# Optimization experiments

Hardware: AMD Instinct MI355X
Metric: run time of the kernel (lower is better)

## Reference

```python
import jax, jax.numpy as jnp
import numpy as np
from jax import lax

B, S, T, E, H, V = 32, 64, 48, 512, 1024, 32000
PAD = 0


def lstm_cell(x, h, c, W_ih, W_hh, b_ih, b_hh):
    # PyTorch gate order: i, f, g, o
    gates = x @ W_ih.T + b_ih + h @ W_hh.T + b_hh
    i, f, g, o = jnp.split(gates, 4, axis=-1)
    c = jax.nn.sigmoid(f) * c + jax.nn.sigmoid(i) * jnp.tanh(g)
    h = jax.nn.sigmoid(o) * jnp.tanh(c)
    return h, c


def setup_inputs() -> dict:
    key = jax.random.key(0)
    ks = jax.random.split(key, 24)
    sc = 0.02
    n = lambda k, shape: jax.random.normal(k, shape, jnp.float32) * sc
    src_emb = n(ks[0], (V, E)).at[PAD].set(0.0)
    tgt_emb = n(ks[1], (V, E)).at[PAD].set(0.0)
    inp = {
        "input_sequences": jax.random.randint(ks[2], (B, S), 0, V),
        "target_sequences": jax.random.randint(ks[3], (B, T), 0, V),
        "src_emb": src_emb,
        "tgt_emb": tgt_emb,
        "enc_Wih_f": n(ks[4], (4 * H, E)),
        "enc_Whh_f": n(ks[5], (4 * H, H)),
        "enc_bih_f": n(ks[6], (4 * H,)),
        "enc_bhh_f": n(ks[7], (4 * H,)),
        "enc_Wih_b": n(ks[8], (4 * H, E)),
        "enc_Whh_b": n(ks[9], (4 * H, H)),
        "enc_bih_b": n(ks[10], (4 * H,)),
        "enc_bhh_b": n(ks[11], (4 * H,)),
        "dec_Wih": n(ks[12], (4 * H, E + H)),
        "dec_Whh": n(ks[13], (4 * H, H)),
        "dec_bih": n(ks[14], (4 * H,)),
        "dec_bhh": n(ks[15], (4 * H,)),
        "W_init_h": n(ks[16], (H, 2 * H)),
        "W_init_c": n(ks[17], (H, 2 * H)),
        "W_att": n(ks[18], (H, 2 * H)),
        "W_comb": n(ks[19], (H, 3 * H)),
        "W_proj": n(ks[20], (V, H)),
    }
    return inp


def reference(input_sequences, target_sequences, src_emb, tgt_emb,
              enc_Wih_f, enc_Whh_f, enc_bih_f, enc_bhh_f,
              enc_Wih_b, enc_Whh_b, enc_bih_b, enc_bhh_b,
              dec_Wih, dec_Whh, dec_bih, dec_bhh,
              W_init_h, W_init_c, W_att, W_comb, W_proj):
    bsz = input_sequences.shape[0]
    x_src = src_emb[input_sequences.T]  # (S, B, E) time-major

    def make_enc_step(W_ih, W_hh, b_ih, b_hh):
        def step(carry, x):
            h, c = carry
            h, c = lstm_cell(x, h, c, W_ih, W_hh, b_ih, b_hh)
            return (h, c), h
        return step

    h0 = jnp.zeros((bsz, H), x_src.dtype)
    c0 = jnp.zeros((bsz, H), x_src.dtype)
    # bidirectional encoder
    (hf, cf), hs_f = lax.scan(make_enc_step(enc_Wih_f, enc_Whh_f, enc_bih_f, enc_bhh_f), (h0, c0), x_src)
    (hb, cb), hs_b = lax.scan(make_enc_step(enc_Wih_b, enc_Whh_b, enc_bih_b, enc_bhh_b), (h0, c0), x_src[::-1])
    enc_h = jnp.concatenate([hs_f, hs_b[::-1]], axis=-1).transpose(1, 0, 2)  # (B, S, 2H)
    last_hidden = jnp.concatenate([hf, hb], axis=-1)  # (B, 2H)
    last_cell = jnp.concatenate([cf, cb], axis=-1)

    dec_h0 = last_hidden @ W_init_h.T
    dec_c0 = last_cell @ W_init_c.T
    enc_att = enc_h @ W_att.T  # (B, S, H)

    x_tgt = tgt_emb[target_sequences.T]  # (T, B, E)

    def dec_step(carry, e_t):
        h, c, prev_out = carry
        x = jnp.concatenate([e_t, prev_out], axis=-1)  # (B, E+H)
        h, c = lstm_cell(x, h, c, dec_Wih, dec_Whh, dec_bih, dec_bhh)
        scores = jnp.einsum('bh,bsh->bs', h, enc_att)
        attn = jax.nn.softmax(scores, axis=-1)
        ctx = jnp.einsum('bs,bsd->bd', attn, enc_h)  # (B, 2H)
        out = jnp.concatenate([h, ctx], axis=-1) @ W_comb.T  # (B, H)
        return (h, c, out), out

    prev0 = jnp.zeros((bsz, H), x_src.dtype)
    _, outs = lax.scan(dec_step, (dec_h0, dec_c0, prev0), x_tgt)  # (T, B, H)

    logits = outs @ W_proj.T  # (T, B, V)
    P = jax.nn.log_softmax(logits, axis=-1)
    tgt = target_sequences.T  # (T, B)
    # P[t] predicts tgt[t+1]; torch.gather with smaller index truncates P to T-1 steps
    gold = jnp.take_along_axis(P[:-1], tgt[1:][..., None], axis=-1)[..., 0]  # (T-1, B)
    scores = gold.sum(axis=0)  # (B,)
    return scores
```

## Files before the change

kernel.cpp:

```cpp
#include <hip/hip_runtime.h>

typedef short v8s __attribute__((ext_vector_type(8)));
typedef float v4f __attribute__((ext_vector_type(4)));
typedef unsigned short u16;

#define DI __device__ __forceinline__
#define MFMA(a, b, c) __builtin_amdgcn_mfma_f32_16x16x32_bf16(a, b, c, 0, 0, 0)

constexpr int B = 32, S = 64, T = 48, E = 512, H = 1024, V = 32000;
constexpr int TP = T - 1;
constexpr int MROWS = TP * B;
constexpr int NCH = 250;

DI u16 f2bf(float f) {
    unsigned u = __float_as_uint(f);
    unsigned r = (u + 0x7FFFu + ((u >> 16) & 1u)) >> 16;
    return (u16)r;
}
DI float bf2f(u16 h) { return __uint_as_float(((unsigned)h) << 16); }
DI v8s load8(const u16* p) { return *reinterpret_cast<const v8s*>(p); }

typedef __attribute__((address_space(1))) const unsigned int gu32;
typedef __attribute__((address_space(3))) unsigned int lu32;
DI void gload_lds16(const u16* g, u16* l) {
    __builtin_amdgcn_global_load_lds((gu32*)g, (lu32*)l, 16, 0, 0);
}

DI void cstore(unsigned* p, unsigned v) {
    __hip_atomic_store(p, v, __ATOMIC_RELAXED, __HIP_MEMORY_SCOPE_AGENT);
}
DI int cload(const int* p) {
    return __hip_atomic_load(p, __ATOMIC_RELAXED, __HIP_MEMORY_SCOPE_AGENT);
}

DI void gbar2(int* bar, int bid, int nblk, int v) {
    __syncthreads();
    if (bid == 0) {
        int t = threadIdx.x;
        if (t > 0 && t < nblk) {
            while (cload(bar + 16 + t * 4) < v) __builtin_amdgcn_s_sleep(1);
        }
        __syncthreads();
        if (t == 0)
            __hip_atomic_store(bar, v, __ATOMIC_RELAXED, __HIP_MEMORY_SCOPE_AGENT);
    } else {
        if (threadIdx.x == 0) {
            __hip_atomic_store(bar + 16 + bid * 4, v, __ATOMIC_RELAXED,
                               __HIP_MEMORY_SCOPE_AGENT);
            while (cload(bar) < v) __builtin_amdgcn_s_sleep(2);
        }
        __syncthreads();
    }
}

__global__ __launch_bounds__(256) void k_cvt(const float* __restrict__ s,
                                             u16* __restrict__ d, int n4) {
    int i = blockIdx.x * 256 + threadIdx.x;
    if (i >= n4) return;
    float4 v = reinterpret_cast<const float4*>(s)[i];
    ushort4 o;
    o.x = f2bf(v.x); o.y = f2bf(v.y); o.z = f2bf(v.z); o.w = f2bf(v.w);
    reinterpret_cast<ushort4*>(d)[i] = o;
}

struct CvtD {
    const float* src[11];
    u16* dst[11];
    int n4[11];
    int start[12];
};
__global__ __launch_bounds__(256) void k_cvtm(CvtD d) {
    int blk = blockIdx.x;
    int seg = 0;
    #pragma unroll
    for (int q = 0; q < 11; ++q)
        if (blk >= d.start[q + 1]) seg = q + 1;
    int i = (blk - d.start[seg]) * 256 + threadIdx.x;
    if (i >= d.n4[seg]) return;
    float4 v = reinterpret_cast<const float4*>(d.src[seg])[i];
    ushort4 o;
    o.x = f2bf(v.x); o.y = f2bf(v.y); o.z = f2bf(v.z); o.w = f2bf(v.w);
    reinterpret_cast<ushort4*>(d.dst[seg])[i] = o;
}

__global__ __launch_bounds__(256) void k_embed(const int* __restrict__ seq, int seqstr,
                                               int nsteps, const float* __restrict__ emb,
                                               u16* __restrict__ out) {
    int i = blockIdx.x * 256 + threadIdx.x;
    int total = nsteps * B * (E / 4);
    if (i >= total) return;
    int q = i & 127;
    int sb = i >> 7;
    int b = sb & 31;
    int s = sb >> 5;
    int tok = seq[b * seqstr + s];
    float4 v = reinterpret_cast<const float4*>(emb + (size_t)tok * E)[q];
    ushort4 o;
    o.x = f2bf(v.x); o.y = f2bf(v.y); o.z = f2bf(v.z); o.w = f2bf(v.w);
    reinterpret_cast<ushort4*>(out + ((size_t)(s * B + b)) * E)[q] = o;
}

__global__ __launch_bounds__(256) void k_ench(const u16* __restrict__ hsf,
                                              const u16* __restrict__ hsb,
                                              u16* __restrict__ ench) {
    int id = blockIdx.x * 256 + threadIdx.x;
    int d8 = id & 255; int s = (id >> 8) & 63; int b = id >> 14;
    int d0 = d8 * 8;
    const u16* src = (d0 < H) ? hsf + (((size_t)(s + 1) * B + b)) * H + d0
                              : hsb + (((size_t)(S - s) * B + b)) * H + (d0 - H);
    *reinterpret_cast<v8s*>(ench + ((size_t)b * S + s) * 2 * H + d0) = load8(src);
}

__global__ __launch_bounds__(256) void k_transp(const u16* __restrict__ in,
                                                u16* __restrict__ out, int K, int N) {
    __shared__ u16 t[64][72];
    int nt = blockIdx.x * 64, kt = blockIdx.y * 64;
    int tid = threadIdx.x;
    int r = tid >> 2, cq = (tid & 3) * 16;
    v8s v0 = load8(in + (size_t)(kt + r) * N + nt + cq);
    v8s v1 = load8(in + (size_t)(kt + r) * N + nt + cq + 8);
    #pragma unroll
    for (int e = 0; e < 8; ++e) { t[r][cq + e] = (u16)v0[e]; t[r][cq + 8 + e] = (u16)v1[e]; }
    __syncthreads();
    v8s o0, o1;
    #pragma unroll
    for (int e = 0; e < 8; ++e) { o0[e] = (short)t[cq + e][r]; o1[e] = (short)t[cq + 8 + e][r]; }
    *reinterpret_cast<v8s*>(out + (size_t)(nt + r) * K + kt + cq) = o0;
    *reinterpret_cast<v8s*>(out + (size_t)(nt + r) * K + kt + cq + 8) = o1;
}

__global__ __launch_bounds__(256) void k_tile(const u16* __restrict__ A, int astr,
                                              const u16* __restrict__ W, int wstr,
                                              float* __restrict__ outf,
                                              u16* __restrict__ outb, int ostr,
                                              int ktiles) {
    __shared__ __align__(16) u16 As[128 * 64];
    __shared__ __align__(16) u16 Bs[128 * 64];
    const int tid = threadIdx.x;
    const int lane = tid & 63, wv = tid >> 6;
    const int l15 = lane & 15, lg = lane >> 4;
    const int wr = wv >> 1, wc = wv & 1;
    const int m0 = blockIdx.y * 128, n0 = blockIdx.x * 128;
    const int srow = lane >> 3, sc_ = lane & 7;

    v4f acc[4][4];
    #pragma unroll
    for (int i = 0; i < 4; ++i)
        #pragma unroll
        for (int j = 0; j < 4; ++j) acc[i][j] = v4f{0.f, 0.f, 0.f, 0.f};

    for (int kt = 0; kt < ktiles; ++kt) {
        const int kb = kt * 64;
        #pragma unroll
        for (int i = 0; i < 4; ++i) {
            int chunk = wv * 4 + i;
            int row = chunk * 8 + srow;
            int csw = (sc_ ^ (row & 7)) << 3;
            gload_lds16(A + (size_t)(m0 + row) * astr + kb + csw, As + chunk * 512);
            gload_lds16(W + (size_t)(n0 + row) * wstr + kb + csw, Bs + chunk * 512);
        }
        __syncthreads();
        #pragma unroll
        for (int kk = 0; kk < 2; ++kk) {
            int sw = (((kk << 2) | lg) ^ (l15 & 7)) << 3;
            v8s af[4], bfv[4];
            #pragma unroll
            for (int mi = 0; mi < 4; ++mi)
                af[mi] = load8(As + (wr * 64 + mi * 16 + l15) * 64 + sw);
            #pragma unroll
            for (int ni = 0; ni < 4; ++ni)
                bfv[ni] = load8(Bs + (wc * 64 + ni * 16 + l15) * 64 + sw);
            #pragma unroll
            for (int mi = 0; mi < 4; ++mi)
                #pragma unroll
                for (int ni = 0; ni < 4; ++ni)
                    acc[mi][ni] = MFMA(af[mi], bfv[ni], acc[mi][ni]);
        }
        __syncthreads();
    }
    #pragma unroll
    for (int mi = 0; mi < 4; ++mi)
        #pragma unroll
        for (int rr = 0; rr < 4; ++rr) {
            int row = m0 + wr * 64 + mi * 16 + lg * 4 + rr;
            #pragma unroll
            for (int ni = 0; ni < 4; ++ni) {
                int col = n0 + wc * 64 + ni * 16 + l15;
                if (outf) outf[(size_t)row * ostr + col] = acc[mi][ni][rr];
                else      outb[(size_t)row * ostr + col] = f2bf(acc[mi][ni][rr]);
            }
        }
}

struct Seg { const u16* a; int astr; const u16* w; int wstr; int k; };

__global__ __launch_bounds__(512) void k_mm(Seg s1, Seg s2, float* __restrict__ outf,
                                            u16* __restrict__ outb, int ostr, int ks) {
    const int tid = threadIdx.x;
    const int wv = tid >> 6, lane = tid & 63;
    const int l15 = lane & 15, lg = lane >> 4;
    const int wrow = blockIdx.x * 16 + l15;
    const int k0 = wv * ks, k1 = k0 + ks;
    v4f acc0 = {0.f, 0.f, 0.f, 0.f}, acc1 = {0.f, 0.f, 0.f, 0.f};
    int base = 0;
    auto doseg = [&](const Seg& sg) {
        if (sg.k == 0) return;
        int s0 = k0 > base ? k0 : base;
        int send = base + sg.k;
        int s1e = k1 < send ? k1 : send;
        const u16* wp = sg.w + (size_t)wrow * sg.wstr + 8 * lg;
        const u16* a0p = sg.a + (size_t)l15 * sg.astr + 8 * lg;
        const u16* a1p = sg.a + (size_t)(16 + l15) * sg.astr + 8 * lg;
        #pragma unroll 2
        for (int k = s0; k < s1e; k += 32) {
            int kl = k - base;
            v8s bf = load8(wp + kl);
            v8s af0 = load8(a0p + kl);
            v8s af1 = load8(a1p + kl);
            acc0 = MFMA(af0, bf, acc0);
            acc1 = MFMA(af1, bf, acc1);
        }
        base += sg.k;
    };
    doseg(s1); doseg(s2);

    __shared__ float g[8][32][16];
    #pragma unroll
    for (int r = 0; r < 4; ++r) {
        g[wv][lg * 4 + r][l15] = acc0[r];
        g[wv][16 + lg * 4 + r][l15] = acc1[r];
    }
    __syncthreads();
    {
        int b = tid >> 4, cl = tid & 15;
        float v = 0.f;
        #pragma unroll
        for (int w = 0; w < 8; ++w) v += g[w][b][cl];
        int col = blockIdx.x * 16 + cl;
        if (outb) outb[(size_t)b * ostr + col] = f2bf(v);
        else      outf[(size_t)b * ostr + col] = v;
    }
}

__global__ __launch_bounds__(512) void k_enc(
    const float* __restrict__ xgF, const float* __restrict__ xgB,
    const u16* __restrict__ whhf, const u16* __restrict__ whhb,
    const float* __restrict__ bihF, const float* __restrict__ bhhF,
    const float* __restrict__ bihB, const float* __restrict__ bhhB,
    u16* __restrict__ hsf, u16* __restrict__ hsb,
    float* __restrict__ cfinal, int* __restrict__ bars) {
    const int blk = blockIdx.x;
    const int dir = blk >> 8, bid = blk & 255;
    const int tid = threadIdx.x;
    const u16* whh = dir ? whhb : whhf;
    const float* xg = dir ? xgB : xgF;
    const float* bih = dir ? bihB : bihF;
    const float* bhh = dir ? bhhB : bhhF;
    u16* hs = dir ? hsb : hsf;
    int* bar = bars + dir * 2048;
    const int j0 = bid * 4;
    __shared__ u16 wlds[16 * 1024];
    __shared__ float glds[8][32][16];
    __shared__ u16 htmp[32][4];
    {
        int r = tid >> 5, kc = tid & 31;
        int gate = r >> 2, jl = r & 3;
        const u16* src = whh + (size_t)(gate * H + j0 + jl) * H;
        #pragma unroll
        for (int i = 0; i < 4; ++i) {
            int c = kc + 32 * i;
            v8s v = load8(src + c * 8);
            *reinterpret_cast<v8s*>(wlds + r * 1024 + ((c ^ (r & 7)) * 8)) = v;
        }
    }
    float creg = 0.f;
    const int pb = tid >> 2, pj = tid & 3;
    float bsum[4];
    if (tid < 128) {
        #pragma unroll
        for (int gt = 0; gt < 4; ++gt)
            bsum[gt] = bih[gt * H + j0 + pj] + bhh[gt * H + j0 + pj];
    }
    __syncthreads();
    const int wv = tid >> 6, lane = tid & 63, l15 = lane & 15, lg = lane >> 4;
    for (int s = 0; s < S; ++s) {
        float xv[4];
        if (tid < 128) {
            int xrow = ((dir ? (S - 1 - s) : s) * 32 + pb) * 4096;
            const float* xr = xg + xrow + j0 + pj;
            #pragma unroll
            for (int gt = 0; gt < 4; ++gt) xv[gt] = xr[gt * H];
        }
        const u16* hp = hs + (size_t)s * (B * H);
        const u16* a0 = hp + (size_t)l15 * H + wv * 128 + 8 * lg;
        const u16* a1 = a0 + (size_t)16 * H;
        v4f acc0 = {0.f, 0.f, 0.f, 0.f}, acc1 = {0.f, 0.f, 0.f, 0.f};
        #pragma unroll
        for (int kb = 0; kb < 4; ++kb) {
            int c = wv * 16 + kb * 4 + lg;
            v8s bf = load8(wlds + l15 * 1024 + ((c ^ (l15 & 7)) * 8));
            v8s af0 = load8(a0 + kb * 32);
            v8s af1 = load8(a1 + kb * 32);
            acc0 = MFMA(af0, bf, acc0);
            acc1 = MFMA(af1, bf, acc1);
        }
        #pragma unroll
        for (int r = 0; r < 4; ++r) {
            glds[wv][lg * 4 + r][l15] = acc0[r];
            glds[wv][16 + lg * 4 + r][l15] = acc1[r];
        }
        __syncthreads();
        if (tid < 128) {
            float gv[4];
            #pragma unroll
            for (int gt = 0; gt < 4; ++gt) {
                float v = 0.f;
                #pragma unroll
                for (int w = 0; w < 8; ++w) v += glds[w][pb][gt * 4 + pj];
                gv[gt] = v + xv[gt] + bsum[gt];
            }
            float si = 1.f / (1.f + expf(-gv[0]));
            float sf = 1.f / (1.f + expf(-gv[1]));
            float tg = tanhf(gv[2]);
            float so = 1.f / (1.f + expf(-gv[3]));
            creg = sf * creg + si * tg;
            htmp[pb][pj] = f2bf(so * tanhf(creg));
        }
        __syncthreads();
        if (tid < 64) {
            int rb = tid >> 1, c2 = (tid & 1) * 2;
            unsigned val = (unsigned)htmp[rb][c2] | ((unsigned)htmp[rb][c2 + 1] << 16);
            cstore((unsigned*)(hs + (size_t)(s + 1) * (B * H) + (size_t)rb * H + j0 + c2), val);
        }
        if (s < S - 1) gbar2(bar, bid, 256, s + 1);
    }
    if (tid < 128) cfinal[(size_t)dir * B * H + (size_t)pb * H + j0 + pj] = creg;
}

__global__ __launch_bounds__(512) void k_dec(
    const float* __restrict__ xgD, const u16* __restrict__ dwhh,
    const u16* __restrict__ wfuse, const float* __restrict__ bih,
    const float* __restrict__ bhh, const float* __restrict__ decc,
    const u16* __restrict__ encab, const u16* __restrict__ ench,
    u16* __restrict__ hc, int* __restrict__ bar) {
    const int bid = blockIdx.x, tid = threadIdx.x;
    const int j0 = bid * 4;
    __shared__ u16 wlds[16 * 3072];
    __shared__ float glds[8][32][16];
    __shared__ float hl[1056];
    __shared__ float sc[64], aw[64];
    __shared__ float cpart[4][128][2];
    __shared__ u16 htmp[32][4];
    {
        int r = tid >> 5, kc = tid & 31;
        int gate = r >> 2, jl = r & 3;
        int grow = gate * H + j0 + jl;
        for (int i = 0; i < 12; ++i) {
            int c = kc + 32 * i;
            int k = c * 8;
            v8s wf = load8(wfuse + (size_t)grow * 3072 + k);
            if (k < 1024) {
                v8s wh = load8(dwhh + (size_t)grow * 1024 + k);
                #pragma unroll
                for (int e = 0; e < 8; ++e)
                    wf[e] = (short)f2bf(bf2f((u16)wf[e]) + bf2f((u16)wh[e]));
            }
            *reinterpret_cast<v8s*>(wlds + r * 3072 + ((c ^ (r & 7)) * 8)) = wf;
        }
    }
    const int pb = tid >> 2, pj = tid & 3;
    float creg = 0.f;
    float bsum[4];
    if (tid < 128) {
        creg = decc[(size_t)pb * H + j0 + pj];
        #pragma unroll
        for (int gt = 0; gt < 4; ++gt)
            bsum[gt] = bih[gt * H + j0 + pj] + bhh[gt * H + j0 + pj];
    }
    __syncthreads();
    const int wv = tid >> 6, lane = tid & 63, l15 = lane & 15, lg = lane >> 4;
    const int ab = bid >> 3, ach = bid & 7;
    for (int t = 0; t < T; ++t) {
        const u16* hp = hc + (size_t)t * (B * 3072);
        u16* hn = hc + (size_t)(t + 1) * (B * 3072);
        float xv[4];
        if (tid < 128) {
            const float* xr = xgD + (size_t)(t * 32 + pb) * 4096 + j0 + pj;
            #pragma unroll
            for (int gt = 0; gt < 4; ++gt) xv[gt] = xr[gt * H];
        }
        const u16* a0 = hp + (size_t)l15 * 3072 + wv * 384 + 8 * lg;
        const u16* a1 = a0 + (size_t)16 * 3072;
        v4f acc0 = {0.f, 0.f, 0.f, 0.f}, acc1 = {0.f, 0.f, 0.f, 0.f};
        #pragma unroll
        for (int kb = 0; kb < 12; ++kb) {
            int c = wv * 48 + kb * 4 + lg;
            v8s bf = load8(wlds + l15 * 3072 + ((c ^ (l15 & 7)) * 8));
            v8s af0 = load8(a0 + kb * 32);
            v8s af1 = load8(a1 + kb * 32);
            acc0 = MFMA(af0, bf, acc0);
            acc1 = MFMA(af1, bf, acc1);
        }
        #pragma unroll
        for (int r = 0; r < 4; ++r) {
            glds[wv][lg * 4 + r][l15] = acc0[r];
            glds[wv][16 + lg * 4 + r][l15] = acc1[r];
        }
        __syncthreads();
        if (tid < 128) {
            float gv[4];
            #pragma unroll
            for (int gt = 0; gt < 4; ++gt) {
                float v = 0.f;
                #pragma unroll
                for (int w = 0; w < 8; ++w) v += glds[w][pb][gt * 4 + pj];
                gv[gt] = v + xv[gt] + bsum[gt];
            }
            float si = 1.f / (1.f + expf(-gv[0]));
            float sf = 1.f / (1.f + expf(-gv[1]));
            float tg = tanhf(gv[2]);
            float so = 1.f / (1.f + expf(-gv[3]));
            creg = sf * creg + si * tg;
            htmp[pb][pj] = f2bf(so * tanhf(creg));
        }
        __syncthreads();
        if (tid < 64) {
            int rb = tid >> 1, c2 = (tid & 1) * 2;
            unsigned val = (unsigned)htmp[rb][c2] | ((unsigned)htmp[rb][c2 + 1] << 16);
            cstore((unsigned*)(hn + (size_t)rb * 3072 + j0 + c2), val);
        }
        gbar2(bar, bid, 256, 2 * t + 1);
        {
            const u16* hb = hn + (size_t)ab * 3072;
            for (int i = tid; i < 1024; i += 512)
                hl[((i >> 7) * 132) + (i & 127)] = bf2f(hb[i]);
            __syncthreads();
            {
                int si2 = tid >> 3, pt = tid & 7;
                const u16* ap = encab + ((size_t)(ab * 64 + si2)) * 1024 + pt * 128;
                const float* hq = hl + pt * 132;
                float ps = 0.f;
                #pragma unroll
                for (int x = 0; x < 16; ++x) {
                    v8s v = load8(ap + x * 8);
                    #pragma unroll
                    for (int e = 0; e < 8; ++e) ps += bf2f((u16)v[e]) * hq[x * 8 + e];
                }
                ps += __shfl_xor(ps, 1); ps += __shfl_xor(ps, 2); ps += __shfl_xor(ps, 4);
                if (pt == 0) sc[si2] = ps;
            }
            __syncthreads();
            if (tid < 64) {
                float v = sc[tid];
                float m = v;
                #pragma unroll
                for (int o = 32; o; o >>= 1) m = fmaxf(m, __shfl_xor(m, o));
                float e = expf(v - m), sum = e;
                #pragma unroll
                for (int o = 32; o; o >>= 1) sum += __shfl_xor(sum, o);
                aw[tid] = e / sum;
            }
            __syncthreads();
            {
                int q = tid >> 7, dp = tid & 127;
                int d = ach * 256 + dp * 2;
                const u16* ep = ench + (size_t)ab * S * 2048 + (size_t)(q * 16) * 2048 + d;
                float c0 = 0.f, c1 = 0.f;
                #pragma unroll 8
                for (int s2 = 0; s2 < 16; ++s2) {
                    unsigned uv = *reinterpret_cast<const unsigned*>(ep);
                    float w = aw[q * 16 + s2];
                    c0 += w * bf2f((u16)(uv & 0xFFFF));
                    c1 += w * bf2f((u16)(uv >> 16));
                    ep += 2048;
                }
                cpart[q][dp][0] = c0;
                cpart[q][dp][1] = c1;
            }
            __syncthreads();
            if (tid < 128) {
                float c0 = cpart[0][tid][0] + cpart[1][tid][0]
                         + cpart[2][tid][0] + cpart[3][tid][0];
                float c1 = cpart[0][tid][1] + cpart[1][tid][1]
                         + cpart[2][tid][1] + cpart[3][tid][1];
                unsigned ov = ((unsigned)f2bf(c1) << 16) | f2bf(c0);
                cstore((unsigned*)(hn + (size_t)ab * 3072 + 1024 + ach * 256 + tid * 2), ov);
            }
        }
        if (t < T - 1) gbar2(bar, bid, 256, 2 * t + 2);
    }
}

__global__ __launch_bounds__(256) void k_sub(float* __restrict__ x,
                                             const float* __restrict__ c) {
    int i = blockIdx.x * 256 + threadIdx.x;
    x[i] -= c[i];
}

__global__ __launch_bounds__(256) void k_hc0(const u16* __restrict__ dech,
                                             u16* __restrict__ hc) {
    int b = blockIdx.x;
    int k = blockIdx.y * 256 + threadIdx.x;
    hc[(size_t)b * 3072 + k] = (k < 1024) ? dech[(size_t)b * 1024 + k] : (u16)0;
}

__global__ __launch_bounds__(512) void k_proj(const u16* __restrict__ A,
                                              const u16* __restrict__ W,
                                              const int* __restrict__ tgt,
                                              float* __restrict__ pmax,
                                              float* __restrict__ psum,
                                              float* __restrict__ pgold) {
    __shared__ __align__(16) u16 As[256 * 64];
    __shared__ __align__(16) u16 Bs[128 * 64];
    __shared__ float red[256][2][3];
    const int tid = threadIdx.x;
    const int lane = tid & 63, wv = tid >> 6;
    const int l15 = lane & 15, lg = lane >> 4;
    const int wr = wv >> 1, wc = wv & 1;
    int orig = blockIdx.x;
    int xcd = orig & 7, loc = orig >> 3;
    int wgid = (xcd < 4 ? xcd * 188 : 752 + (xcd - 4) * 187) + loc;
    int nt = wgid / 6, mt = wgid % 6;
    const int m0 = mt * 256, n0 = nt * 128;
    const int srow = lane >> 3, sc_ = lane & 7;

    v4f acc[4][4];
    #pragma unroll
    for (int i = 0; i < 4; ++i)
        #pragma unroll
        for (int j = 0; j < 4; ++j) acc[i][j] = v4f{0.f, 0.f, 0.f, 0.f};

    for (int kt = 0; kt < 16; ++kt) {
        const int kb = kt * 64;
        #pragma unroll
        for (int i = 0; i < 4; ++i) {
            int chunk = wv * 4 + i;
            int row = chunk * 8 + srow;
            int csw = (sc_ ^ (row & 7)) << 3;
            gload_lds16(A + (size_t)(m0 + row) * 1024 + kb + csw, As + chunk * 512);
        }
        #pragma unroll
        for (int i = 0; i < 2; ++i) {
            int chunk = wv * 2 + i;
            int row = chunk * 8 + srow;
            int csw = (sc_ ^ (row & 7)) << 3;
            gload_lds16(W + (size_t)(n0 + row) * 1024 + kb + csw, Bs + chunk * 512);
        }
        __syncthreads();
        #pragma unroll
        for (int kk = 0; kk < 2; ++kk) {
            int sw = (((kk << 2) | lg) ^ (l15 & 7)) << 3;
            v8s af[4], bfv[4];
            #pragma unroll
            for (int mi = 0; mi < 4; ++mi)
                af[mi] = load8(As + (wr * 64 + mi * 16 + l15) * 64 + sw);
            #pragma unroll
            for (int ni = 0; ni < 4; ++ni)
                bfv[ni] = load8(Bs + (wc * 64 + ni * 16 + l15) * 64 + sw);
            #pragma unroll
            for (int mi = 0; mi < 4; ++mi)
                #pragma unroll
                for (int ni = 0; ni < 4; ++ni)
                    acc[mi][ni] = MFMA(af[mi], bfv[ni], acc[mi][ni]);
        }
        __syncthreads();
    }
    #pragma unroll
    for (int mi = 0; mi < 4; ++mi) {
        #pragma unroll
        for (int rr = 0; rr < 4; ++rr) {
            int lrow = wr * 64 + mi * 16 + lg * 4 + rr;
            int grow = m0 + lrow;
            float vmax = -1e30f;
            #pragma unroll
            for (int ni = 0; ni < 4; ++ni) vmax = fmaxf(vmax, acc[mi][ni][rr]);
            #pragma unroll
            for (int x = 1; x < 16; x <<= 1) vmax = fmaxf(vmax, __shfl_xor(vmax, x));
            float se = 0.f;
            #pragma unroll
            for (int ni = 0; ni < 4; ++ni) se += expf(acc[mi][ni][rr] - vmax);
            #pragma unroll
            for (int x = 1; x < 16; x <<= 1) se += __shfl_xor(se, x);
            int t = grow >> 5, b = grow & 31;
            int g = (grow < MROWS) ? tgt[b * T + t + 1] : -1;
            float gv = 0.f;
            #pragma unroll
            for (int ni = 0; ni < 4; ++ni) {
                int col = n0 + wc * 64 + ni * 16 + l15;
                if (col == g) gv = acc[mi][ni][rr];
            }
            #pragma unroll
            for (int x = 1; x < 16; x <<= 1) gv += __shfl_xor(gv, x);
            if (l15 == 0) {
                red[lrow][wc][0] = vmax;
                red[lrow][wc][1] = se;
                red[lrow][wc][2] = gv;
            }
        }
    }
    __syncthreads();
    if (tid < 256) {
        int grow = m0 + tid;
        if (grow < MROWS) {
            float ma = red[tid][0][0], mb = red[tid][1][0];
            float M = fmaxf(ma, mb);
            float Sv = red[tid][0][1] * expf(ma - M) + red[tid][1][1] * expf(mb - M);
            float G = red[tid][0][2] + red[tid][1][2];
            size_t idx = (size_t)grow * NCH + nt;
            pmax[idx] = M; psum[idx] = Sv; pgold[idx] = G;
        }
    }
}

__global__ __launch_bounds__(256) void k_lse(const float* __restrict__ pmax,
                                             const float* __restrict__ psum,
                                             const float* __restrict__ pgold,
                                             float* __restrict__ logP) {
    int item = blockIdx.x * 4 + (threadIdx.x >> 6);
    int lane = threadIdx.x & 63;
    if (item >= MROWS) return;
    float m = -1e30f, g = 0.f;
    for (int c = lane; c < NCH; c += 64) {
        size_t idx = (size_t)item * NCH + c;
        m = fmaxf(m, pmax[idx]);
        g += pgold[idx];
    }
    for (int o = 32; o; o >>= 1) m = fmaxf(m, __shfl_xor(m, o));
    float s = 0.f;
    for (int c = lane; c < NCH; c += 64) {
        size_t idx = (size_t)item * NCH + c;
        s += psum[idx] * expf(pmax[idx] - m);
    }
    for (int o = 32; o; o >>= 1) { s += __shfl_xor(s, o); g += __shfl_xor(g, o); }
    if (lane == 0) logP[item] = g - (m + logf(s));
}

__global__ __launch_bounds__(64) void k_final(const float* __restrict__ logP,
                                              float* __restrict__ out) {
    int b = threadIdx.x;
    if (b < 32) {
        float s = 0.f;
        for (int t = 0; t < TP; ++t) s += logP[t * 32 + b];
        out[b] = s;
    }
}

extern "C" void kernel_launch(void* const* d_in, const int* in_sizes, int n_in,
                              void* d_out, int out_size, void* d_ws, size_t ws_size,
                              hipStream_t stream) {
    const int*   seq_in  = (const int*)d_in[0];
    const int*   seq_tgt = (const int*)d_in[1];
    const float* src_emb = (const float*)d_in[2];
    const float* tgt_emb = (const float*)d_in[3];
    const float* eWihF = (const float*)d_in[4];
    const float* eWhhF = (const float*)d_in[5];
    const float* eBihF = (const float*)d_in[6];
    const float* eBhhF = (const float*)d_in[7];
    const float* eWihB = (const float*)d_in[8];
    const float* eWhhB = (const float*)d_in[9];
    const float* eBihB = (const float*)d_in[10];
    const float* eBhhB = (const float*)d_in[11];
    const float* dWih  = (const float*)d_in[12];
    const float* dWhh  = (const float*)d_in[13];
    const float* dBih  = (const float*)d_in[14];
    const float* dBhh  = (const float*)d_in[15];
    const float* WinH  = (const float*)d_in[16];
    const float* WinC  = (const float*)d_in[17];
    const float* Watt  = (const float*)d_in[18];
    const float* Wcomb = (const float*)d_in[19];
    const float* Wproj = (const float*)d_in[20];

    char* ws = (char*)d_ws;
    size_t off = 0;
    auto alloc = [&](size_t bytes) -> char* {
        off = (off + 255) & ~(size_t)255;
        char* p = ws + off;
        off += bytes;
        return p;
    };
    const size_t G4 = 4 * (size_t)H;
    const size_t slot = (size_t)B * H;
    u16* wihf = (u16*)alloc(G4 * E * 2);
    u16* whhf = (u16*)alloc(G4 * H * 2);
    u16* wihb = (u16*)alloc(G4 * E * 2);
    u16* whhb = (u16*)alloc(G4 * H * 2);
    u16* dwih = (u16*)alloc(G4 * (E + H) * 2);
    u16* dwhh = (u16*)alloc(G4 * H * 2);
    u16* winh = (u16*)alloc((size_t)H * 2 * H * 2);
    u16* winc = (u16*)alloc((size_t)H * 2 * H * 2);
    u16* watt = (u16*)alloc((size_t)H * 2 * H * 2);
    u16* wcmb = (u16*)alloc((size_t)H * 3 * H * 2);
    u16* wprj = (u16*)alloc((size_t)V * H * 2);
    u16* wcmbT = (u16*)alloc((size_t)3 * H * H * 2);
    u16* wfuse = (u16*)alloc((size_t)G4 * 3 * H * 2);
    u16* xsrc  = (u16*)alloc((size_t)S * B * E * 2);
    u16* xtgt  = (u16*)alloc((size_t)T * B * E * 2);
    u16* hsf   = (u16*)alloc((size_t)(S + 1) * slot * 2);
    u16* hsb   = (u16*)alloc((size_t)(S + 1) * slot * 2);
    u16* ench  = (u16*)alloc((size_t)B * S * 2 * H * 2);
    u16* encab = (u16*)alloc((size_t)B * S * H * 2);
    u16* dech  = (u16*)alloc(slot * 2);
    u16* hc    = (u16*)alloc((size_t)(T + 1) * B * 3072 * 2);
    u16* outsb = (u16*)alloc((size_t)(T * B) * H * 2);
    u16* lcbf  = (u16*)alloc(2 * slot * 2);
    float* xgF  = (float*)alloc((size_t)S * B * G4 * 4);
    float* xgB  = (float*)alloc((size_t)S * B * G4 * 4);
    float* xgD  = (float*)alloc((size_t)T * B * G4 * 4);
    float* cf2  = (float*)alloc(2 * slot * 4);
    float* decc = (float*)alloc(slot * 4);
    float* corr = (float*)alloc((size_t)B * G4 * 4);
    float* pmax  = (float*)alloc((size_t)MROWS * NCH * 4);
    float* psum  = (float*)alloc((size_t)MROWS * NCH * 4);
    float* pgold = (float*)alloc((size_t)MROWS * NCH * 4);
    float* logP  = (float*)alloc((size_t)MROWS * 4);
    int* bars = (int*)alloc(3 * 2048 * 4);
    (void)ws_size; (void)in_sizes; (void)n_in; (void)out_size;

    hipMemsetAsync(hsf, 0, slot * 2, stream);
    hipMemsetAsync(hsb, 0, slot * 2, stream);
    hipMemsetAsync(bars, 0, 3 * 2048 * 4, stream);

    {
        CvtD d;
        const float* srcs[11] = {eWihF, eWhhF, eWihB, eWhhB, dWih, dWhh,
                                 WinH, WinC, Watt, Wcomb, Wproj};
        u16* dsts[11] = {wihf, whhf, wihb, whhb, dwih, dwhh,
                         winh, winc, watt, wcmb, wprj};
        size_t ns[11] = {G4 * E, G4 * H, G4 * E, G4 * H, G4 * (E + H), G4 * H,
                         (size_t)H * 2 * H, (size_t)H * 2 * H, (size_t)H * 2 * H,
                         (size_t)H * 3 * H, (size_t)V * H};
        int blk = 0;
        for (int i = 0; i < 11; ++i) {
            d.src[i] = srcs[i];
            d.dst[i] = dsts[i];
            d.n4[i] = (int)(ns[i] / 4);
            d.start[i] = blk;
            blk += (d.n4[i] + 255) / 256;
        }
        d.start[11] = blk;
        k_cvtm<<<dim3(blk), dim3(256), 0, stream>>>(d);
    }

    k_embed<<<dim3((S * B * (E / 4) + 255) / 256), dim3(256), 0, stream>>>(
        seq_in, S, S, src_emb, xsrc);
    k_embed<<<dim3((T * B * (E / 4) + 255) / 256), dim3(256), 0, stream>>>(
        seq_tgt, T, T, tgt_emb, xtgt);

    k_transp<<<dim3(3 * H / 64, H / 64), dim3(256), 0, stream>>>(wcmb, wcmbT, H, 3 * H);

    k_tile<<<dim3(32, 16), dim3(256), 0, stream>>>(xsrc, E, wihf, E, xgF, nullptr, 4096, 8);
    k_tile<<<dim3(32, 16), dim3(256), 0, stream>>>(xsrc, E, wihb, E, xgB, nullptr, 4096, 8);
    k_tile<<<dim3(32, 12), dim3(256), 0, stream>>>(xtgt, E, dwih, E + H, xgD, nullptr, 4096, 8);
    k_tile<<<dim3(24, 32), dim3(256), 0, stream>>>(dwih + E, E + H, wcmbT, H,
                                                   nullptr, wfuse, 3 * H, 16);

    k_enc<<<dim3(512), dim3(512), 0, stream>>>(xgF, xgB, whhf, whhb,
                                               eBihF, eBhhF, eBihB, eBhhB,
                                               hsf, hsb, cf2, bars);

    k_ench<<<dim3(B * S * (2 * H / 8) / 256), dim3(256), 0, stream>>>(hsf, hsb, ench);
    k_tile<<<dim3(8, 16), dim3(256), 0, stream>>>(ench, 2 * H, watt, 2 * H,
                                                  nullptr, encab, H, 32);
    {
        int n4 = (int)(2 * slot / 4);
        k_cvt<<<dim3((n4 + 255) / 256), dim3(256), 0, stream>>>(cf2, lcbf, n4);
    }

    {
        Seg a1{hsf + (size_t)S * slot, H, winh, 2 * H, H};
        Seg a2{hsb + (size_t)S * slot, H, winh + H, 2 * H, H};
        k_mm<<<dim3(H / 16), dim3(512), 0, stream>>>(a1, a2, nullptr, dech, H, 2 * H / 8);
        Seg c1{lcbf, H, winc, 2 * H, H};
        Seg c2{lcbf + slot, H, winc + H, 2 * H, H};
        k_mm<<<dim3(H / 16), dim3(512), 0, stream>>>(c1, c2, decc, nullptr, H, 2 * H / 8);
        Seg f1{dech, H, wfuse, 3 * H, H};
        Seg f0{nullptr, 0, nullptr, 0, 0};
        k_mm<<<dim3(G4 / 16), dim3(512), 0, stream>>>(f1, f0, corr, nullptr, 4096, H / 8);
        k_sub<<<dim3(B * G4 / 256), dim3(256), 0, stream>>>(xgD, corr);
        k_hc0<<<dim3(B, 12), dim3(256), 0, stream>>>(dech, hc);
    }

    k_dec<<<dim3(256), dim3(512), 0, stream>>>(xgD, dwhh, wfuse, dBih, dBhh, decc,
                                               encab, ench, hc, bars + 4096);

    k_tile<<<dim3(8, 12), dim3(256), 0, stream>>>(hc + B * 3072, 3 * H, wcmb, 3 * H,
                                                  nullptr, outsb, H, 48);

    k_proj<<<dim3(1500), dim3(512), 0, stream>>>(outsb, wprj, seq_tgt, pmax, psum, pgold);
    k_lse<<<dim3((MROWS + 3) / 4), dim3(256), 0, stream>>>(pmax, psum, pgold, logP);
    k_final<<<dim3(1), dim3(64), 0, stream>>>(logP, (float*)d_out);
}
```

Before: 1.420 ms.

## Halve persistent recurrent grids, keep weight tiles in registers, fuse init kernels

The encoder and decoder persistent kernels now give each block 8 hidden units instead of 4. The grids are halved to 256 and 128 blocks, and the recurrent weight slices are held in VGPRs instead of LDS. Each wave now issues four MFMAs per k-step, and the grid barrier spans half as many blocks, which should cut per-step barrier latency. The k_sub and k_hc0 launches are folded into k_mm through a subtract mode and a direct write into hc. The tradeoffs are more register pressure (24 v8s of weights in the decoder) and fewer CUs doing the per-step work.

```diff
diff --git a/kernel.cpp b/kernel.cpp
--- a/kernel.cpp
+++ b/kernel.cpp
@@ -195,7 +195,8 @@
 struct Seg { const u16* a; int astr; const u16* w; int wstr; int k; };
 
 __global__ __launch_bounds__(512) void k_mm(Seg s1, Seg s2, float* __restrict__ outf,
-                                            u16* __restrict__ outb, int ostr, int ks) {
+                                            u16* __restrict__ outb, int ostr, int ks,
+                                            int sub) {
     const int tid = threadIdx.x;
     const int wv = tid >> 6, lane = tid & 63;
     const int l15 = lane & 15, lg = lane >> 4;
@@ -237,8 +238,10 @@
         #pragma unroll
         for (int w = 0; w < 8; ++w) v += g[w][b][cl];
         int col = blockIdx.x * 16 + cl;
-        if (outb) outb[(size_t)b * ostr + col] = f2bf(v);
-        else      outf[(size_t)b * ostr + col] = v;
+        size_t idx = (size_t)b * ostr + col;
+        if (outb)      outb[idx] = f2bf(v);
+        else if (sub)  outf[idx] -= v;
+        else           outf[idx] = v;
     }
 }
 
@@ -250,7 +253,7 @@
     u16* __restrict__ hsf, u16* __restrict__ hsb,
     float* __restrict__ cfinal, int* __restrict__ bars) {
     const int blk = blockIdx.x;
-    const int dir = blk >> 8, bid = blk & 255;
+    const int dir = blk >> 7, bid = blk & 127;
     const int tid = threadIdx.x;
     const u16* whh = dir ? whhb : whhf;
     const float* xg = dir ? xgB : xgF;
@@ -258,34 +261,30 @@
     const float* bhh = dir ? bhhB : bhhF;
     u16* hs = dir ? hsb : hsf;
     int* bar = bars + dir * 2048;
-    const int j0 = bid * 4;
-    __shared__ u16 wlds[16 * 1024];
-    __shared__ float glds[8][32][16];
-    __shared__ u16 htmp[32][4];
-    {
-        int r = tid >> 5, kc = tid & 31;
-        int gate = r >> 2, jl = r & 3;
-        const u16* src = whh + (size_t)(gate * H + j0 + jl) * H;
-        #pragma unroll
-        for (int i = 0; i < 4; ++i) {
-            int c = kc + 32 * i;
-            v8s v = load8(src + c * 8);
-            *reinterpret_cast<v8s*>(wlds + r * 1024 + ((c ^ (r & 7)) * 8)) = v;
-        }
-    }
+    const int j0 = bid * 8;
+    __shared__ float glds[8][32][34];
+    __shared__ u16 htmp[32][8];
+    const int wv = tid >> 6, lane = tid & 63, l15 = lane & 15, lg = lane >> 4;
+    v8s wreg[2][4];
+    #pragma unroll
+    for (int rt = 0; rt < 2; ++rt) {
+        int wrow = rt * 16 + l15;
+        int grow = (wrow >> 3) * H + j0 + (wrow & 7);
+        #pragma unroll
+        for (int kb = 0; kb < 4; ++kb)
+            wreg[rt][kb] = load8(whh + (size_t)grow * H + wv * 128 + kb * 32 + lg * 8);
+    }
+    const int pb = tid >> 3, pj = tid & 7;
     float creg = 0.f;
-    const int pb = tid >> 2, pj = tid & 3;
     float bsum[4];
-    if (tid < 128) {
+    if (tid < 256) {
         #pragma unroll
         for (int gt = 0; gt < 4; ++gt)
             bsum[gt] = bih[gt * H + j0 + pj] + bhh[gt * H + j0 + pj];
     }
-    __syncthreads();
-    const int wv = tid >> 6, lane = tid & 63, l15 = lane & 15, lg = lane >> 4;
     for (int s = 0; s < S; ++s) {
         float xv[4];
-        if (tid < 128) {
+        if (tid < 256) {
             int xrow = ((dir ? (S - 1 - s) : s) * 32 + pb) * 4096;
             const float* xr = xg + xrow + j0 + pj;
             #pragma unroll
@@ -294,29 +293,31 @@
         const u16* hp = hs + (size_t)s * (B * H);
         const u16* a0 = hp + (size_t)l15 * H + wv * 128 + 8 * lg;
         const u16* a1 = a0 + (size_t)16 * H;
-        v4f acc0 = {0.f, 0.f, 0.f, 0.f}, acc1 = {0.f, 0.f, 0.f, 0.f};
+        v4f acc00 = {0,0,0,0}, acc01 = {0,0,0,0}, acc10 = {0,0,0,0}, acc11 = {0,0,0,0};
         #pragma unroll
         for (int kb = 0; kb < 4; ++kb) {
-            int c = wv * 16 + kb * 4 + lg;
-            v8s bf = load8(wlds + l15 * 1024 + ((c ^ (l15 & 7)) * 8));
             v8s af0 = load8(a0 + kb * 32);
             v8s af1 = load8(a1 + kb * 32);
-            acc0 = MFMA(af0, bf, acc0);
-            acc1 = MFMA(af1, bf, acc1);
+            acc00 = MFMA(af0, wreg[0][kb], acc00);
+            acc10 = MFMA(af0, wreg[1][kb], acc10);
+            acc01 = MFMA(af1, wreg[0][kb], acc01);
+            acc11 = MFMA(af1, wreg[1][kb], acc11);
         }
         #pragma unroll
         for (int r = 0; r < 4; ++r) {
-            glds[wv][lg * 4 + r][l15] = acc0[r];
-            glds[wv][16 + lg * 4 + r][l15] = acc1[r];
-        }
-        __syncthreads();
-        if (tid < 128) {
+            glds[wv][lg * 4 + r][l15] = acc00[r];
+            glds[wv][lg * 4 + r][16 + l15] = acc10[r];
+            glds[wv][16 + lg * 4 + r][l15] = acc01[r];
+            glds[wv][16 + lg * 4 + r][16 + l15] = acc11[r];
+        }
+        __syncthreads();
+        if (tid < 256) {
             float gv[4];
             #pragma unroll
             for (int gt = 0; gt < 4; ++gt) {
                 float v = 0.f;
                 #pragma unroll
-                for (int w = 0; w < 8; ++w) v += glds[w][pb][gt * 4 + pj];
+                for (int w = 0; w < 8; ++w) v += glds[w][pb][gt * 8 + pj];
                 gv[gt] = v + xv[gt] + bsum[gt];
             }
             float si = 1.f / (1.f + expf(-gv[0]));
@@ -327,14 +328,14 @@
             htmp[pb][pj] = f2bf(so * tanhf(creg));
         }
         __syncthreads();
-        if (tid < 64) {
-            int rb = tid >> 1, c2 = (tid & 1) * 2;
+        if (tid < 128) {
+            int rb = tid >> 2, c2 = (tid & 3) * 2;
             unsigned val = (unsigned)htmp[rb][c2] | ((unsigned)htmp[rb][c2 + 1] << 16);
             cstore((unsigned*)(hs + (size_t)(s + 1) * (B * H) + (size_t)rb * H + j0 + c2), val);
         }
-        if (s < S - 1) gbar2(bar, bid, 256, s + 1);
-    }
-    if (tid < 128) cfinal[(size_t)dir * B * H + (size_t)pb * H + j0 + pj] = creg;
+        if (s < S - 1) gbar2(bar, bid, 128, s + 1);
+    }
+    if (tid < 256) cfinal[(size_t)dir * B * H + (size_t)pb * H + j0 + pj] = creg;
 }
 
 __global__ __launch_bounds__(512) void k_dec(
@@ -344,76 +345,77 @@
     const u16* __restrict__ encab, const u16* __restrict__ ench,
     u16* __restrict__ hc, int* __restrict__ bar) {
     const int bid = blockIdx.x, tid = threadIdx.x;
-    const int j0 = bid * 4;
-    __shared__ u16 wlds[16 * 3072];
-    __shared__ float glds[8][32][16];
+    const int j0 = bid * 8;
+    __shared__ float glds[8][32][34];
     __shared__ float hl[1056];
     __shared__ float sc[64], aw[64];
-    __shared__ float cpart[4][128][2];
-    __shared__ u16 htmp[32][4];
-    {
-        int r = tid >> 5, kc = tid & 31;
-        int gate = r >> 2, jl = r & 3;
-        int grow = gate * H + j0 + jl;
-        for (int i = 0; i < 12; ++i) {
-            int c = kc + 32 * i;
-            int k = c * 8;
+    __shared__ float cpart[2][256][2];
+    __shared__ u16 htmp[32][8];
+    const int wv = tid >> 6, lane = tid & 63, l15 = lane & 15, lg = lane >> 4;
+    v8s wreg[2][12];
+    #pragma unroll
+    for (int rt = 0; rt < 2; ++rt) {
+        int wrow = rt * 16 + l15;
+        int grow = (wrow >> 3) * H + j0 + (wrow & 7);
+        #pragma unroll
+        for (int kb = 0; kb < 12; ++kb) {
+            int k = wv * 384 + kb * 32 + lg * 8;
             v8s wf = load8(wfuse + (size_t)grow * 3072 + k);
-            if (k < 1024) {
+            if (wv * 384 + kb * 32 < 1024) {
                 v8s wh = load8(dwhh + (size_t)grow * 1024 + k);
                 #pragma unroll
                 for (int e = 0; e < 8; ++e)
                     wf[e] = (short)f2bf(bf2f((u16)wf[e]) + bf2f((u16)wh[e]));
             }
-            *reinterpret_cast<v8s*>(wlds + r * 3072 + ((c ^ (r & 7)) * 8)) = wf;
-        }
-    }
-    const int pb = tid >> 2, pj = tid & 3;
+            wreg[rt][kb] = wf;
+        }
+    }
+    const int pb = tid >> 3, pj = tid & 7;
     float creg = 0.f;
     float bsum[4];
-    if (tid < 128) {
+    if (tid < 256) {
         creg = decc[(size_t)pb * H + j0 + pj];
         #pragma unroll
         for (int gt = 0; gt < 4; ++gt)
             bsum[gt] = bih[gt * H + j0 + pj] + bhh[gt * H + j0 + pj];
     }
-    __syncthreads();
-    const int wv = tid >> 6, lane = tid & 63, l15 = lane & 15, lg = lane >> 4;
-    const int ab = bid >> 3, ach = bid & 7;
+    const int ab = bid >> 2, ach = bid & 3;
     for (int t = 0; t < T; ++t) {
         const u16* hp = hc + (size_t)t * (B * 3072);
         u16* hn = hc + (size_t)(t + 1) * (B * 3072);
         float xv[4];
-        if (tid < 128) {
+        if (tid < 256) {
             const float* xr = xgD + (size_t)(t * 32 + pb) * 4096 + j0 + pj;
             #pragma unroll
             for (int gt = 0; gt < 4; ++gt) xv[gt] = xr[gt * H];
         }
         const u16* a0 = hp + (size_t)l15 * 3072 + wv * 384 + 8 * lg;
         const u16* a1 = a0 + (size_t)16 * 3072;
-        v4f acc0 = {0.f, 0.f, 0.f, 0.f}, acc1 = {0.f, 0.f, 0.f, 0.f};
+        v4f acc00 = {0,0,0,0}, acc01 = {0,0,0,0}, acc10 = {0,0,0,0}, acc11 = {0,0,0,0};
         #pragma unroll
         for (int kb = 0; kb < 12; ++kb) {
-            int c = wv * 48 + kb * 4 + lg;
-            v8s bf = load8(wlds + l15 * 3072 + ((c ^ (l15 & 7)) * 8));
             v8s af0 = load8(a0 + kb * 32);
             v8s af1 = load8(a1 + kb * 32);
-            acc0 = MFMA(af0, bf, acc0);
-            acc1 = MFMA(af1, bf, acc1);
+            acc00 = MFMA(af0, wreg[0][kb], acc00);
+            acc10 = MFMA(af0, wreg[1][kb], acc10);
+            acc01 = MFMA(af1, wreg[0][kb], acc01);
+            acc11 = MFMA(af1, wreg[1][kb], acc11);
         }
         #pragma unroll
         for (int r = 0; r < 4; ++r) {
-            glds[wv][lg * 4 + r][l15] = acc0[r];
-            glds[wv][16 + lg * 4 + r][l15] = acc1[r];
-        }
-        __syncthreads();
-        if (tid < 128) {
+            glds[wv][lg * 4 + r][l15] = acc00[r];
+            glds[wv][lg * 4 + r][16 + l15] = acc10[r];
+            glds[wv][16 + lg * 4 + r][l15] = acc01[r];
+            glds[wv][16 + lg * 4 + r][16 + l15] = acc11[r];
+        }
+        __syncthreads();
+        if (tid < 256) {
             float gv[4];
             #pragma unroll
             for (int gt = 0; gt < 4; ++gt) {
                 float v = 0.f;
                 #pragma unroll
-                for (int w = 0; w < 8; ++w) v += glds[w][pb][gt * 4 + pj];
+                for (int w = 0; w < 8; ++w) v += glds[w][pb][gt * 8 + pj];
                 gv[gt] = v + xv[gt] + bsum[gt];
             }
             float si = 1.f / (1.f + expf(-gv[0]));
@@ -424,12 +426,12 @@
             htmp[pb][pj] = f2bf(so * tanhf(creg));
         }
         __syncthreads();
-        if (tid < 64) {
-            int rb = tid >> 1, c2 = (tid & 1) * 2;
+        if (tid < 128) {
+            int rb = tid >> 2, c2 = (tid & 3) * 2;
             unsigned val = (unsigned)htmp[rb][c2] | ((unsigned)htmp[rb][c2 + 1] << 16);
             cstore((unsigned*)(hn + (size_t)rb * 3072 + j0 + c2), val);
         }
-        gbar2(bar, bid, 256, 2 * t + 1);
+        gbar2(bar, bid, 128, 2 * t + 1);
         {
             const u16* hb = hn + (size_t)ab * 3072;
             for (int i = tid; i < 1024; i += 512)
@@ -462,14 +464,14 @@
             }
             __syncthreads();
             {
-                int q = tid >> 7, dp = tid & 127;
-                int d = ach * 256 + dp * 2;
-                const u16* ep = ench + (size_t)ab * S * 2048 + (size_t)(q * 16) * 2048 + d;
+                int q = tid >> 8, dp = tid & 255;
+                int d = ach * 512 + dp * 2;
+                const u16* ep = ench + (size_t)ab * S * 2048 + (size_t)(q * 32) * 2048 + d;
                 float c0 = 0.f, c1 = 0.f;
                 #pragma unroll 8
-                for (int s2 = 0; s2 < 16; ++s2) {
+                for (int s2 = 0; s2 < 32; ++s2) {
                     unsigned uv = *reinterpret_cast<const unsigned*>(ep);
-                    float w = aw[q * 16 + s2];
+                    float w = aw[q * 32 + s2];
                     c0 += w * bf2f((u16)(uv & 0xFFFF));
                     c1 += w * bf2f((u16)(uv >> 16));
                     ep += 2048;
@@ -478,30 +480,15 @@
                 cpart[q][dp][1] = c1;
             }
             __syncthreads();
-            if (tid < 128) {
-                float c0 = cpart[0][tid][0] + cpart[1][tid][0]
-                         + cpart[2][tid][0] + cpart[3][tid][0];
-                float c1 = cpart[0][tid][1] + cpart[1][tid][1]
-                         + cpart[2][tid][1] + cpart[3][tid][1];
+            if (tid < 256) {
+                float c0 = cpart[0][tid][0] + cpart[1][tid][0];
+                float c1 = cpart[0][tid][1] + cpart[1][tid][1];
                 unsigned ov = ((unsigned)f2bf(c1) << 16) | f2bf(c0);
-                cstore((unsigned*)(hn + (size_t)ab * 3072 + 1024 + ach * 256 + tid * 2), ov);
-            }
-        }
-        if (t < T - 1) gbar2(bar, bid, 256, 2 * t + 2);
-    }
-}
-
-__global__ __launch_bounds__(256) void k_sub(float* __restrict__ x,
-                                             const float* __restrict__ c) {
-    int i = blockIdx.x * 256 + threadIdx.x;
-    x[i] -= c[i];
-}
-
-__global__ __launch_bounds__(256) void k_hc0(const u16* __restrict__ dech,
-                                             u16* __restrict__ hc) {
-    int b = blockIdx.x;
-    int k = blockIdx.y * 256 + threadIdx.x;
-    hc[(size_t)b * 3072 + k] = (k < 1024) ? dech[(size_t)b * 1024 + k] : (u16)0;
+                cstore((unsigned*)(hn + (size_t)ab * 3072 + 1024 + ach * 512 + tid * 2), ov);
+            }
+        }
+        if (t < T - 1) gbar2(bar, bid, 128, 2 * t + 2);
+    }
 }
 
 __global__ __launch_bounds__(512) void k_proj(const u16* __restrict__ A,
@@ -699,7 +686,6 @@
     u16* hsb   = (u16*)alloc((size_t)(S + 1) * slot * 2);
     u16* ench  = (u16*)alloc((size_t)B * S * 2 * H * 2);
     u16* encab = (u16*)alloc((size_t)B * S * H * 2);
-    u16* dech  = (u16*)alloc(slot * 2);
     u16* hc    = (u16*)alloc((size_t)(T + 1) * B * 3072 * 2);
     u16* outsb = (u16*)alloc((size_t)(T * B) * H * 2);
     u16* lcbf  = (u16*)alloc(2 * slot * 2);
@@ -708,7 +694,6 @@
     float* xgD  = (float*)alloc((size_t)T * B * G4 * 4);
     float* cf2  = (float*)alloc(2 * slot * 4);
     float* decc = (float*)alloc(slot * 4);
-    float* corr = (float*)alloc((size_t)B * G4 * 4);
     float* pmax  = (float*)alloc((size_t)MROWS * NCH * 4);
     float* psum  = (float*)alloc((size_t)MROWS * NCH * 4);
     float* pgold = (float*)alloc((size_t)MROWS * NCH * 4);
@@ -718,6 +703,7 @@
 
     hipMemsetAsync(hsf, 0, slot * 2, stream);
     hipMemsetAsync(hsb, 0, slot * 2, stream);
+    hipMemsetAsync(hc, 0, (size_t)B * 3072 * 2, stream);
     hipMemsetAsync(bars, 0, 3 * 2048 * 4, stream);
 
     {
@@ -754,7 +740,7 @@
     k_tile<<<dim3(24, 32), dim3(256), 0, stream>>>(dwih + E, E + H, wcmbT, H,
                                                    nullptr, wfuse, 3 * H, 16);
 
-    k_enc<<<dim3(512), dim3(512), 0, stream>>>(xgF, xgB, whhf, whhb,
+    k_enc<<<dim3(256), dim3(512), 0, stream>>>(xgF, xgB, whhf, whhb,
                                                eBihF, eBhhF, eBihB, eBhhB,
                                                hsf, hsb, cf2, bars);
 
@@ -769,18 +755,19 @@
     {
         Seg a1{hsf + (size_t)S * slot, H, winh, 2 * H, H};
         Seg a2{hsb + (size_t)S * slot, H, winh + H, 2 * H, H};
-        k_mm<<<dim3(H / 16), dim3(512), 0, stream>>>(a1, a2, nullptr, dech, H, 2 * H / 8);
+        k_mm<<<dim3(H / 16), dim3(512), 0, stream>>>(a1, a2, nullptr, hc, 3072,
+                                                     2 * H / 8, 0);
         Seg c1{lcbf, H, winc, 2 * H, H};
         Seg c2{lcbf + slot, H, winc + H, 2 * H, H};
-        k_mm<<<dim3(H / 16), dim3(512), 0, stream>>>(c1, c2, decc, nullptr, H, 2 * H / 8);
-        Seg f1{dech, H, wfuse, 3 * H, H};
+        k_mm<<<dim3(H / 16), dim3(512), 0, stream>>>(c1, c2, decc, nullptr, H,
+                                                     2 * H / 8, 0);
+        Seg f1{hc, 3072, wfuse, 3 * H, H};
         Seg f0{nullptr, 0, nullptr, 0, 0};
-        k_mm<<<dim3(G4 / 16), dim3(512), 0, stream>>>(f1, f0, corr, nullptr, 4096, H / 8);
-        k_sub<<<dim3(B * G4 / 256), dim3(256), 0, stream>>>(xgD, corr);
-        k_hc0<<<dim3(B, 12), dim3(256), 0, stream>>>(dech, hc);
-    }
-
-    k_dec<<<dim3(256), dim3(512), 0, stream>>>(xgD, dwhh, wfuse, dBih, dBhh, decc,
+        k_mm<<<dim3(G4 / 16), dim3(512), 0, stream>>>(f1, f0, xgD, nullptr, 4096,
+                                                      H / 8, 1);
+    }
+
+    k_dec<<<dim3(128), dim3(512), 0, stream>>>(xgD, dwhh, wfuse, dBih, dBhh, decc,
                                                encab, ench, hc, bars + 4096);
 
     k_tile<<<dim3(8, 12), dim3(256), 0, stream>>>(hc + B * 3072, 3 * H, wcmb, 3 * H,
```

Result: slower. 2.209 ms (+55.5%).
